# Optimization experiments

Hardware: AMD Instinct MI355X
Metric: run time of the kernel (lower is better)

Reference implementation:

```python
import jax, jax.numpy as jnp
import numpy as np

N_NODES = 100000
N_EDGES = 1600000
N_GRAPHS = 1024
IN_FEATS = 74
HID = 100


def setup_inputs() -> dict:
    key = jax.random.key(0)
    ks = jax.random.split(key, 16)
    node_feats = jax.random.normal(ks[0], (N_NODES, IN_FEATS), dtype=jnp.float32)
    src = jax.random.randint(ks[1], (N_EDGES,), 0, N_NODES, dtype=jnp.int32)
    dst = jax.random.randint(ks[2], (N_EDGES,), 0, N_NODES, dtype=jnp.int32)
    graph_ids = jnp.sort(jax.random.randint(ks[3], (N_NODES,), 0, N_GRAPHS, dtype=jnp.int32))

    def lin(k, fi, fo):
        s = 1.0 / np.sqrt(fi)
        kw, kb = jax.random.split(k)
        return (jax.random.uniform(kw, (fi, fo), jnp.float32, -s, s),
                jax.random.uniform(kb, (fo,), jnp.float32, -s, s))

    W_self1, _ = lin(ks[4], IN_FEATS, HID)
    W_neigh1, b1 = lin(ks[5], IN_FEATS, HID)
    W_self2, _ = lin(ks[6], HID, HID)
    W_neigh2, b2 = lin(ks[7], HID, HID)
    w_atom, b_atom = lin(ks[8], HID, 1)
    W_p1, b_p1 = lin(ks[9], 2 * HID, 64)
    W_p2, b_p2 = lin(ks[10], 64, 1)
    return {
        'node_feats': node_feats, 'src': src, 'dst': dst, 'graph_ids': graph_ids,
        'n_graphs': N_GRAPHS,
        'W_self1': W_self1, 'W_neigh1': W_neigh1, 'b1': b1,
        'W_self2': W_self2, 'W_neigh2': W_neigh2, 'b2': b2,
        'w_atom': w_atom, 'b_atom': b_atom,
        'W_p1': W_p1, 'b_p1': b_p1, 'W_p2': W_p2, 'b_p2': b_p2,
    }


def _sage_mean_layer(h, src, dst, W_self, W_neigh, b):
    # DGL SAGEConv, aggregator 'mean': out = h @ W_self + mean_{u->v}(h_u) @ W_neigh + b
    n = h.shape[0]
    msg = h[src]  # [E, F] gather
    agg = jax.ops.segment_sum(msg, dst, num_segments=n)
    deg = jax.ops.segment_sum(jnp.ones((src.shape[0],), h.dtype), dst, num_segments=n)
    h_neigh = agg / jnp.maximum(deg, 1.0)[:, None]
    return jax.nn.relu(h @ W_self + h_neigh @ W_neigh + b)


def reference(node_feats, src, dst, graph_ids, n_graphs,
              W_self1, W_neigh1, b1, W_self2, W_neigh2, b2,
              w_atom, b_atom, W_p1, b_p1, W_p2, b_p2):
    h = _sage_mean_layer(node_feats, src, dst, W_self1, W_neigh1, b1)
    h = _sage_mean_layer(h, src, dst, W_self2, W_neigh2, b2)

    # WeightedSumAndMax readout
    w = jax.nn.sigmoid(h @ w_atom + b_atom)          # [N, 1]
    g_sum = jax.ops.segment_sum(h * w, graph_ids, num_segments=n_graphs)   # [G, HID]
    g_max = jax.ops.segment_max(h, graph_ids, num_segments=n_graphs)       # [G, HID]
    g_max = jnp.where(jnp.isneginf(g_max), 0.0, g_max)  # empty graphs -> 0
    g_feats = jnp.concatenate([g_sum, g_max], axis=-1)  # [G, 2*HID]

    # MLP predictor: Linear(200,64) -> Linear(64,1) (no activation between)
    out = (g_feats @ W_p1 + b_p1) @ W_p2 + b_p2
    return out
```

## Files before the change

### kernel.cpp

```cpp
#include <hip/hip_runtime.h>

#define N_NODES 100000
#define N_PAD   100096
#define N_EDGES 1600000
#define N_GRAPHS 1024
#define F_IN 74
#define HID 100

#define KP1 160
#define KP2 224

#define FBF_LD 80
#define F8T_LD 80
#define AGT_LD 80
#define AGT2_LD 112
#define H1C8_LD 128
#define H2_LD  100

#define ZROW N_NODES

#define NB ((N_NODES + 255) / 256)
#define BKCAP 8192
#define BIN_EPB 4096
#define NBB ((N_EDGES + BIN_EPB - 1) / BIN_EPB)

typedef __attribute__((ext_vector_type(8))) short short8;
typedef __attribute__((ext_vector_type(4))) float f32x4;
typedef __attribute__((ext_vector_type(2))) float f32x2;

#if defined(__has_builtin)
#if __has_builtin(__builtin_amdgcn_cvt_pk_f32_fp8) && __has_builtin(__builtin_amdgcn_cvt_pk_fp8_f32)
#define HAVE_FP8 1
#endif
#endif

__device__ __forceinline__ unsigned short f2bf(float x) {
    union { float f; unsigned u; } c; c.f = x;
    unsigned u = c.u;
    unsigned r = (u + 0x7fffu + ((u >> 16) & 1u)) >> 16;
    return (unsigned short)r;
}
__device__ __forceinline__ float bf2f(unsigned short h) {
    union { unsigned u; float f; } c; c.u = ((unsigned)h) << 16;
    return c.f;
}
__device__ __forceinline__ float blo(unsigned w) { return bf2f((unsigned short)(w & 0xffffu)); }
__device__ __forceinline__ float bhi(unsigned w) { return bf2f((unsigned short)(w >> 16)); }
__device__ __forceinline__ unsigned bpack(float a, float b) {
    return (unsigned)f2bf(a) | ((unsigned)f2bf(b) << 16);
}
__device__ __forceinline__ void store8(void* p, unsigned lo, unsigned hi) {
    unsigned long long v = (unsigned long long)lo | ((unsigned long long)hi << 32);
    *(unsigned long long*)p = v;
}

__device__ __forceinline__ unsigned char enc_fp8_1(float v) {
#ifdef HAVE_FP8
    return (unsigned char)__builtin_amdgcn_cvt_pk_fp8_f32(v, 0.f, 0, false);
#else
    unsigned sgn = v < 0.f ? 0x80u : 0u;
    float m = fabsf(v);
    unsigned char mag;
    if (m < 0.015625f) {
        int q = (int)(m * 512.0f + 0.5f);
        mag = (unsigned char)(q > 7 ? 7 : q);
    } else {
        union { float f; unsigned u; } c; c.f = m;
        unsigned r = c.u + 0x7ffff + ((c.u >> 20) & 1u);
        int e = (int)(r >> 23) - 127;
        mag = (e > 8) ? (unsigned char)0x7e : (unsigned char)(((e + 7) << 3) | ((r >> 20) & 7u));
    }
    return (unsigned char)(sgn | mag);
#endif
}
__device__ __forceinline__ unsigned enc_fp8x4(float v0, float v1, float v2, float v3) {
#ifdef HAVE_FP8
    int r = __builtin_amdgcn_cvt_pk_fp8_f32(v0, v1, 0, false);
    r = __builtin_amdgcn_cvt_pk_fp8_f32(v2, v3, r, true);
    return (unsigned)r;
#else
    return (unsigned)enc_fp8_1(v0) | ((unsigned)enc_fp8_1(v1) << 8) |
           ((unsigned)enc_fp8_1(v2) << 16) | ((unsigned)enc_fp8_1(v3) << 24);
#endif
}
__device__ __forceinline__ void dec_fp8x4(unsigned w, float& x0, float& x1, float& x2, float& x3) {
#ifdef HAVE_FP8
    f32x2 lo = __builtin_amdgcn_cvt_pk_f32_fp8((int)w, false);
    f32x2 hi = __builtin_amdgcn_cvt_pk_f32_fp8((int)w, true);
    x0 = lo.x; x1 = lo.y; x2 = hi.x; x3 = hi.y;
#else
    auto d1 = [](unsigned b) -> float {
        float s = (b & 0x80u) ? -1.f : 1.f;
        b &= 0x7fu;
        if (b < 8) return s * (float)b * 0.001953125f;
        union { unsigned u; float f; } c;
        c.u = ((((b >> 3) & 15u) - 7 + 127) << 23) | ((b & 7u) << 20);
        return s * c.f;
    };
    x0 = d1(w & 0xffu); x1 = d1((w >> 8) & 0xffu);
    x2 = d1((w >> 16) & 0xffu); x3 = d1(w >> 24);
#endif
}
__device__ __forceinline__ short8 dec8bf(uint2 v) {
    float x0, x1, x2, x3, y0, y1, y2, y3;
    dec_fp8x4(v.x, x0, x1, x2, x3);
    dec_fp8x4(v.y, y0, y1, y2, y3);
    union { short8 s; unsigned u[4]; } r;
    r.u[0] = bpack(x0, x1); r.u[1] = bpack(x2, x3);
    r.u[2] = bpack(y0, y1); r.u[3] = bpack(y2, y3);
    return r.s;
}


__global__ __launch_bounds__(256) void k_bin(const int* __restrict__ src,
                                             const int* __restrict__ dst,
                                             int* __restrict__ bucket_fill,
                                             unsigned* __restrict__ bbuf) {
    __shared__ int cnt[NB];
    __shared__ int base[NB];
    int t = threadIdx.x;
    for (int i = t; i < NB; i += 256) cnt[i] = 0;
    __syncthreads();
    int e0 = blockIdx.x * BIN_EPB;
    int e1 = e0 + BIN_EPB < N_EDGES ? e0 + BIN_EPB : N_EDGES;
    for (int e = e0 + t; e < e1; e += 256) {
        atomicAdd(&cnt[dst[e] >> 8], 1);
    }
    __syncthreads();
    for (int i = t; i < NB; i += 256) {
        int c = cnt[i];
        base[i] = c ? atomicAdd(&bucket_fill[i], c) : 0;
        cnt[i] = 0;
    }
    __syncthreads();
    for (int e = e0 + t; e < e1; e += 256) {
        int d = dst[e];
        int b = d >> 8;
        int pos = atomicAdd(&cnt[b], 1);
        bbuf[(size_t)b * BKCAP + base[b] + pos] = ((unsigned)src[e] << 8) | (unsigned)(d & 255);
    }
}

__global__ __launch_bounds__(256) void k_scatter(const unsigned* __restrict__ bbuf,
                                                 const int* __restrict__ bucket_fill,
                                                 int2* __restrict__ rp2,
                                                 int* __restrict__ csr) {
    __shared__ int fc[256];
    __shared__ int ofs[256];
    __shared__ int wsum[4];
    int b = blockIdx.x, t = threadIdx.x;
    int nstart = b << 8;
    int base = b * BKCAP;
    int bend = base + bucket_fill[b];
    fc[t] = 0;
    __syncthreads();
    for (int i = base + t; i < bend; i += 256)
        atomicAdd(&fc[bbuf[i] & 255u], 1);
    __syncthreads();
    int d = fc[t];
    int dp = (d + 7) & ~7;
    int lane = t & 63, w = t >> 6;
    int inc = dp;
    #pragma unroll
    for (int o = 1; o < 64; o <<= 1) {
        int x = __shfl_up(inc, o, 64);
        if (lane >= o) inc += x;
    }
    if (lane == 63) wsum[w] = inc;
    __syncthreads();
    int woff = 0;
    for (int i = 0; i < w; ++i) woff += wsum[i];
    ofs[t] = base + woff + inc - dp;
    __syncthreads();
    int node = nstart + t;
    int o0 = ofs[t];
    if (node < N_NODES) rp2[node] = make_int2(o0, o0 + d);
    for (int i = o0 + d; i < o0 + dp; ++i) csr[i] = ZROW;
    fc[t] = 0;
    __syncthreads();
    for (int i = base + t; i < bend; i += 256) {
        unsigned p = bbuf[i];
        int dl = (int)(p & 255u);
        int pos = atomicAdd(&fc[dl], 1);
        csr[ofs[dl] + pos] = (int)(p >> 8);
    }
}


__global__ void k_feats(const float* __restrict__ feats, short* __restrict__ fbf,
                        unsigned* __restrict__ f8t, unsigned* __restrict__ h1c8) {
    int idx = blockIdx.x * blockDim.x + threadIdx.x;
    if (idx < H1C8_LD / 4) h1c8[(size_t)ZROW * (H1C8_LD / 4) + idx] = 0u;
    if (idx >= (N_NODES + 1) * (F8T_LD / 4)) return;
    int n = idx / (F8T_LD / 4), g = idx - n * (F8T_LD / 4);
    int c0 = 4 * g;
    float v0 = 0.f, v1 = 0.f, v2 = 0.f, v3 = 0.f;
    if (n < N_NODES) {
        const float* r = feats + (size_t)n * F_IN;
        v0 = (c0 + 0 < F_IN) ? r[c0 + 0] : 0.f;
        v1 = (c0 + 1 < F_IN) ? r[c0 + 1] : 0.f;
        v2 = (c0 + 2 < F_IN) ? r[c0 + 2] : 0.f;
        v3 = (c0 + 3 < F_IN) ? r[c0 + 3] : 0.f;
    }
    unsigned* fb = (unsigned*)fbf + (size_t)n * (FBF_LD / 2) + 2 * g;
    fb[0] = bpack(v0, v1);
    fb[1] = bpack(v2, v3);
    f8t[idx] = enc_fp8x4(v0, v1, v2, v3);
}


template <int KP, int K1, int AGG0>
__global__ void k_wconv(const float* __restrict__ Ws, const float* __restrict__ Wn,
                        short* __restrict__ Whi, short* __restrict__ Wlo) {
    int idx = blockIdx.x * blockDim.x + threadIdx.x;
    if (idx >= 112 * KP) return;
    int col = idx / KP, k = idx - col * KP;
    float v = 0.f;
    if (col < HID) {
        if (k < K1) v = Ws[k * HID + col];
        else if (k >= AGG0 && k < AGG0 + K1) v = Wn[(k - AGG0) * HID + col];
    }
    unsigned short hi = f2bf(v);
    unsigned short lo = f2bf(v - bf2f(hi));
    Whi[idx] = (short)hi;
    Wlo[idx] = (short)lo;
}


__global__ __launch_bounds__(256) void k_prep1(const unsigned char* __restrict__ f8t,
                        const int2* __restrict__ rp2, const int* __restrict__ csr,
                        short* __restrict__ agt) {
    int wid = threadIdx.x >> 6, lane = threadIdx.x & 63;
    int v = blockIdx.x * 4 + wid;
    if (v >= N_NODES) return;
    int h = lane >> 5, q = lane & 31;
    int2 se = rp2[v];
    int s = se.x, e = se.y;
    int deg = e - s;
    int pe = s + ((deg + 7) & ~7);
    float a0 = 0.f, a1 = 0.f, a2 = 0.f, a3 = 0.f;
    if (q < 19) {
        #pragma unroll 2
        for (int j = s; j < pe; j += 8) {
            unsigned w0 = *(const unsigned*)(f8t + (size_t)csr[j + h] * F8T_LD + q * 4);
            unsigned w1 = *(const unsigned*)(f8t + (size_t)csr[j + 2 + h] * F8T_LD + q * 4);
            unsigned w2 = *(const unsigned*)(f8t + (size_t)csr[j + 4 + h] * F8T_LD + q * 4);
            unsigned w3 = *(const unsigned*)(f8t + (size_t)csr[j + 6 + h] * F8T_LD + q * 4);
            float x0, x1, x2, x3;
            dec_fp8x4(w0, x0, x1, x2, x3); a0 += x0; a1 += x1; a2 += x2; a3 += x3;
            dec_fp8x4(w1, x0, x1, x2, x3); a0 += x0; a1 += x1; a2 += x2; a3 += x3;
            dec_fp8x4(w2, x0, x1, x2, x3); a0 += x0; a1 += x1; a2 += x2; a3 += x3;
            dec_fp8x4(w3, x0, x1, x2, x3); a0 += x0; a1 += x1; a2 += x2; a3 += x3;
        }
    }
    a0 += __shfl_xor(a0, 32, 64);
    a1 += __shfl_xor(a1, 32, 64);
    a2 += __shfl_xor(a2, 32, 64);
    a3 += __shfl_xor(a3, 32, 64);
    float inv = 1.0f / fmaxf((float)deg, 1.0f);
    if (h == 0 && q < 20) {
        store8((char*)agt + (size_t)v * (AGT_LD * 2) + q * 8,
               bpack(a0 * inv, a1 * inv), bpack(a2 * inv, a3 * inv));
    }
}


__global__ __launch_bounds__(256) void k_prep2(const unsigned char* __restrict__ h1c8,
                        const int2* __restrict__ rp2, const int* __restrict__ csr,
                        short* __restrict__ agt2) {
    int wid = threadIdx.x >> 6, lane = threadIdx.x & 63;
    int v = blockIdx.x * 4 + wid;
    if (v >= N_NODES) return;
    int h = lane >> 5, q = lane & 31;
    int2 se = rp2[v];
    int s = se.x, e = se.y;
    int deg = e - s;
    int pe = s + ((deg + 7) & ~7);
    float a0 = 0.f, a1 = 0.f, a2 = 0.f, a3 = 0.f;
    if (q < 25) {
        #pragma unroll 2
        for (int j = s; j < pe; j += 8) {
            unsigned w0 = *(const unsigned*)(h1c8 + (size_t)csr[j + h] * H1C8_LD + q * 4);
            unsigned w1 = *(const unsigned*)(h1c8 + (size_t)csr[j + 2 + h] * H1C8_LD + q * 4);
            unsigned w2 = *(const unsigned*)(h1c8 + (size_t)csr[j + 4 + h] * H1C8_LD + q * 4);
            unsigned w3 = *(const unsigned*)(h1c8 + (size_t)csr[j + 6 + h] * H1C8_LD + q * 4);
            float x0, x1, x2, x3;
            dec_fp8x4(w0, x0, x1, x2, x3); a0 += x0; a1 += x1; a2 += x2; a3 += x3;
            dec_fp8x4(w1, x0, x1, x2, x3); a0 += x0; a1 += x1; a2 += x2; a3 += x3;
            dec_fp8x4(w2, x0, x1, x2, x3); a0 += x0; a1 += x1; a2 += x2; a3 += x3;
            dec_fp8x4(w3, x0, x1, x2, x3); a0 += x0; a1 += x1; a2 += x2; a3 += x3;
        }
    }
    a0 += __shfl_xor(a0, 32, 64);
    a1 += __shfl_xor(a1, 32, 64);
    a2 += __shfl_xor(a2, 32, 64);
    a3 += __shfl_xor(a3, 32, 64);
    float inv = 1.0f / fmaxf((float)deg, 1.0f);
    char* Aw = (char*)agt2 + (size_t)v * (AGT2_LD * 2);
    if (h == 0 && q < 25) {
        store8(Aw + q * 8, bpack(a0 * inv, a1 * inv), bpack(a2 * inv, a3 * inv));
    }
    if (h == 1 && q < 3) {
        store8(Aw + 200 + q * 8, 0u, 0u);
    }
}


__global__ __launch_bounds__(128) void k_mfma1(
    const short* __restrict__ fbf, const short* __restrict__ agt,
    const short* __restrict__ Wthi, const short* __restrict__ Wtlo,
    const float* __restrict__ bias, unsigned char* __restrict__ h1c8) {
    int t = threadIdx.x;
    int wid = t >> 6, lane = t & 63;
    int quad = lane >> 4, lr = lane & 15;
    int rowbase = blockIdx.x * 64 + wid * 32;

    short8 ap[2][5];
    #pragma unroll
    for (int rf = 0; rf < 2; ++rf) {
        int row = rowbase + rf * 16 + lr;
        #pragma unroll
        for (int c = 0; c < 5; ++c) {
            const short* p;
            if (c < 2) p = fbf + (size_t)row * FBF_LD + c * 32 + quad * 8;
            else if (c == 2) p = (quad < 2) ? fbf + (size_t)row * FBF_LD + 64 + quad * 8
                                            : agt + (size_t)row * AGT_LD + (quad - 2) * 8;
            else p = agt + (size_t)row * AGT_LD + (c - 3) * 32 + 16 + quad * 8;
            ap[rf][c] = *(const short8*)p;
        }
    }

    f32x4 acc[2][7];
    #pragma unroll
    for (int rf = 0; rf < 2; ++rf)
        #pragma unroll
        for (int n = 0; n < 7; ++n) acc[rf][n] = (f32x4){0.f, 0.f, 0.f, 0.f};

    #pragma unroll
    for (int c = 0; c < 5; ++c) {
        #pragma unroll
        for (int n = 0; n < 7; ++n) {
            size_t off = (size_t)(n * 16 + lr) * KP1 + c * 32 + quad * 8;
            short8 wh = *(const short8*)(Wthi + off);
            short8 wl = *(const short8*)(Wtlo + off);
            #pragma unroll
            for (int rf = 0; rf < 2; ++rf) {
                acc[rf][n] = __builtin_amdgcn_mfma_f32_16x16x32_bf16(ap[rf][c], wh, acc[rf][n], 0, 0, 0);
                acc[rf][n] = __builtin_amdgcn_mfma_f32_16x16x32_bf16(ap[rf][c], wl, acc[rf][n], 0, 0, 0);
            }
        }
    }

    #pragma unroll
    for (int rf = 0; rf < 2; ++rf) {
        #pragma unroll
        for (int n = 0; n < 7; ++n) {
            int col = n * 16 + lr;
            float bv = (col < HID) ? bias[col] : 0.f;
            #pragma unroll
            for (int r = 0; r < 4; ++r) {
                int row = rowbase + rf * 16 + quad * 4 + r;
                if (row < N_NODES) {
                    unsigned char enc = 0;
                    if (col < HID) enc = enc_fp8_1(fmaxf(acc[rf][n][r] + bv, 0.f));
                    h1c8[(size_t)row * H1C8_LD + col] = enc;
                }
            }
        }
        #pragma unroll
        for (int r = 0; r < 4; ++r) {
            int row = rowbase + rf * 16 + quad * 4 + r;
            if (row < N_NODES) h1c8[(size_t)row * H1C8_LD + 112 + lr] = 0;
        }
    }
}


__global__ __launch_bounds__(128) void k_mfma2(
    const unsigned char* __restrict__ h1c8, const short* __restrict__ agt2,
    const short* __restrict__ Wthi, const short* __restrict__ Wtlo,
    const float* __restrict__ bias, const float* __restrict__ w_atom,
    const float* __restrict__ b_atom,
    short* __restrict__ h2c, float* __restrict__ aw) {
    int t = threadIdx.x;
    int wid = t >> 6, lane = t & 63;
    int quad = lane >> 4, lr = lane & 15;
    int rowbase = blockIdx.x * 64 + wid * 32;

    short8 ap[2][7];
    #pragma unroll
    for (int rf = 0; rf < 2; ++rf) {
        int row = rowbase + rf * 16 + lr;
        const unsigned char* hr = h1c8 + (size_t)row * H1C8_LD;
        const short* ar = agt2 + (size_t)row * AGT2_LD;
        #pragma unroll
        for (int c = 0; c < 7; ++c) {
            if (c < 3) {
                ap[rf][c] = dec8bf(*(const uint2*)(hr + c * 32 + quad * 8));
            } else if (c == 3) {
                if (quad < 2) ap[rf][c] = dec8bf(*(const uint2*)(hr + 96 + quad * 8));
                else ap[rf][c] = *(const short8*)(ar + (quad - 2) * 8);
            } else {
                ap[rf][c] = *(const short8*)(ar + (c - 4) * 32 + 16 + quad * 8);
            }
        }
    }

    f32x4 acc[2][7];
    #pragma unroll
    for (int rf = 0; rf < 2; ++rf)
        #pragma unroll
        for (int n = 0; n < 7; ++n) acc[rf][n] = (f32x4){0.f, 0.f, 0.f, 0.f};

    #pragma unroll
    for (int c = 0; c < 7; ++c) {
        #pragma unroll
        for (int n = 0; n < 7; ++n) {
            size_t off = (size_t)(n * 16 + lr) * KP2 + c * 32 + quad * 8;
            short8 wh = *(const short8*)(Wthi + off);
            short8 wl = *(const short8*)(Wtlo + off);
            #pragma unroll
            for (int rf = 0; rf < 2; ++rf) {
                acc[rf][n] = __builtin_amdgcn_mfma_f32_16x16x32_bf16(ap[rf][c], wh, acc[rf][n], 0, 0, 0);
                acc[rf][n] = __builtin_amdgcn_mfma_f32_16x16x32_bf16(ap[rf][c], wl, acc[rf][n], 0, 0, 0);
            }
        }
    }

    float ba = b_atom[0];
    #pragma unroll
    for (int rf = 0; rf < 2; ++rf) {
        float dotr0 = 0.f, dotr1 = 0.f, dotr2 = 0.f, dotr3 = 0.f;
        #pragma unroll
        for (int n = 0; n < 7; ++n) {
            int col = n * 16 + lr;
            if (col < HID) {
                float bv = bias[col];
                float wa = w_atom[col];
                #pragma unroll
                for (int r = 0; r < 4; ++r) {
                    int row = rowbase + rf * 16 + quad * 4 + r;
                    if (row < N_NODES) {
                        float v = fmaxf(acc[rf][n][r] + bv, 0.f);
                        h2c[(size_t)row * H2_LD + col] = (short)f2bf(v);
                        float dv = v * wa;
                        if (r == 0) dotr0 += dv;
                        else if (r == 1) dotr1 += dv;
                        else if (r == 2) dotr2 += dv;
                        else dotr3 += dv;
                    }
                }
            }
        }
        #pragma unroll
        for (int off = 1; off < 16; off <<= 1) {
            dotr0 += __shfl_xor(dotr0, off, 64);
            dotr1 += __shfl_xor(dotr1, off, 64);
            dotr2 += __shfl_xor(dotr2, off, 64);
            dotr3 += __shfl_xor(dotr3, off, 64);
        }
        if (lr == 0) {
            int row0 = rowbase + rf * 16 + quad * 4;
            float d[4] = {dotr0, dotr1, dotr2, dotr3};
            #pragma unroll
            for (int r = 0; r < 4; ++r) {
                int row = row0 + r;
                if (row < N_NODES) aw[row] = 1.f / (1.f + __expf(-(d[r] + ba)));
            }
        }
    }
}


__global__ void k_weff(const float* __restrict__ Wp1, const float* __restrict__ bp1,
                       const float* __restrict__ Wp2, const float* __restrict__ bp2,
                       float* __restrict__ weff) {
    int t = threadIdx.x;
    if (t < 200) {
        float s = 0.f;
        for (int k = 0; k < 64; ++k) s += Wp1[t * 64 + k] * Wp2[k];
        weff[t] = s;
    } else if (t == 200) {
        float s = bp2[0];
        for (int k = 0; k < 64; ++k) s += bp1[k] * Wp2[k];
        weff[200] = s;
    }
}


__global__ __launch_bounds__(256) void k_readout(
    const unsigned short* __restrict__ h2c, const float* __restrict__ aw,
    const int* __restrict__ graph_ids, const float* __restrict__ weff,
    float* __restrict__ out) {
    int g = blockIdx.x;
    int t = threadIdx.x, lane = t & 63, w = t >> 6;

    int s_, e_;
    {
        int l = 0, r = N_NODES;
        while (l < r) { int m = (l + r) >> 1; if (graph_ids[m] < g) l = m + 1; else r = m; }
        s_ = l;
        l = s_; r = N_NODES;
        while (l < r) { int m = (l + r) >> 1; if (graph_ids[m] < g + 1) l = m + 1; else r = m; }
        e_ = l;
    }

    float sum0 = 0.f, sum1 = 0.f, mx0 = 0.f, mx1 = 0.f;
    for (int i = s_ + w; i < e_; i += 4) {
        float wt = aw[i];
        if (lane < 50) {
            unsigned wv = *(const unsigned*)(h2c + (size_t)i * H2_LD + 2 * lane);
            float v0 = blo(wv), v1 = bhi(wv);
            sum0 += v0 * wt;
            sum1 += v1 * wt;
            mx0 = fmaxf(mx0, v0);
            mx1 = fmaxf(mx1, v1);
        }
    }

    __shared__ float ssum[4][HID];
    __shared__ float smx[4][HID];
    if (lane < 50) {
        ssum[w][2 * lane] = sum0;
        ssum[w][2 * lane + 1] = sum1;
        smx[w][2 * lane] = mx0;
        smx[w][2 * lane + 1] = mx1;
    }
    __syncthreads();

    float contrib = 0.f;
    if (t < HID) {
        float sumf = ssum[0][t] + ssum[1][t] + ssum[2][t] + ssum[3][t];
        float mxf = fmaxf(fmaxf(smx[0][t], smx[1][t]), fmaxf(smx[2][t], smx[3][t]));
        contrib = sumf * weff[t] + mxf * weff[HID + t];
    }
    #pragma unroll
    for (int off = 32; off; off >>= 1) contrib += __shfl_xor(contrib, off, 64);
    __shared__ float red[4];
    if (lane == 0) red[w] = contrib;
    __syncthreads();
    if (t == 0) out[g] = red[0] + red[1] + red[2] + red[3] + weff[200];
}


extern "C" void kernel_launch(void* const* d_in, const int* in_sizes, int n_in,
                              void* d_out, int out_size, void* d_ws, size_t ws_size,
                              hipStream_t stream) {
    const float* node_feats = (const float*)d_in[0];
    const int* src = (const int*)d_in[1];
    const int* dst = (const int*)d_in[2];
    const int* gid = (const int*)d_in[3];
    const float* Ws1 = (const float*)d_in[5];
    const float* Wn1 = (const float*)d_in[6];
    const float* b1 = (const float*)d_in[7];
    const float* Ws2 = (const float*)d_in[8];
    const float* Wn2 = (const float*)d_in[9];
    const float* b2 = (const float*)d_in[10];
    const float* w_atom = (const float*)d_in[11];
    const float* b_atom = (const float*)d_in[12];
    const float* Wp1 = (const float*)d_in[13];
    const float* bp1 = (const float*)d_in[14];
    const float* Wp2 = (const float*)d_in[15];
    const float* bp2 = (const float*)d_in[16];
    float* out = (float*)d_out;

    char* ws = (char*)d_ws;
    size_t off = 0;
    auto alloc = [&](size_t bytes) -> void* {
        void* p = (void*)(ws + off);
        off += (bytes + 255) & ~(size_t)255;
        return p;
    };
    int2* rp2 = (int2*)alloc((size_t)N_NODES * sizeof(int2));
    int* bucket_fill = (int*)alloc(NB * sizeof(int));
    int* csr = (int*)alloc((size_t)NB * BKCAP * sizeof(int));
    unsigned* bbuf = (unsigned*)alloc((size_t)NB * BKCAP * sizeof(unsigned));
    short* fbf = (short*)alloc((size_t)(N_PAD + 1) * FBF_LD * sizeof(short));
    unsigned char* f8t = (unsigned char*)alloc((size_t)(N_PAD + 1) * F8T_LD);
    short* agt = (short*)alloc((size_t)N_PAD * AGT_LD * sizeof(short));
    short* agt2 = (short*)alloc((size_t)N_PAD * AGT2_LD * sizeof(short));
    unsigned char* h1c8 = (unsigned char*)alloc((size_t)(N_NODES + 1) * H1C8_LD);
    short* h2c = (short*)alloc((size_t)N_NODES * H2_LD * sizeof(short));
    float* aw = (float*)alloc((size_t)N_NODES * sizeof(float));
    short* Wt1hi = (short*)alloc(112 * KP1 * sizeof(short));
    short* Wt1lo = (short*)alloc(112 * KP1 * sizeof(short));
    short* Wt2hi = (short*)alloc(112 * KP2 * sizeof(short));
    short* Wt2lo = (short*)alloc(112 * KP2 * sizeof(short));
    float* weff = (float*)alloc(256 * sizeof(float));

    hipMemsetAsync(bucket_fill, 0, NB * sizeof(int), stream);

    k_bin<<<NBB, 256, 0, stream>>>(src, dst, bucket_fill, bbuf);
    k_scatter<<<NB, 256, 0, stream>>>(bbuf, bucket_fill, rp2, csr);

    k_feats<<<((N_NODES + 1) * (F8T_LD / 4) + 255) / 256, 256, 0, stream>>>(
        node_feats, fbf, (unsigned*)f8t, (unsigned*)h1c8);
    k_wconv<KP1, F_IN, 80><<<(112 * KP1 + 255) / 256, 256, 0, stream>>>(Ws1, Wn1, Wt1hi, Wt1lo);
    k_wconv<KP2, HID, 112><<<(112 * KP2 + 255) / 256, 256, 0, stream>>>(Ws2, Wn2, Wt2hi, Wt2lo);

    k_prep1<<<(N_NODES + 3) / 4, 256, 0, stream>>>(f8t, rp2, csr, agt);
    k_mfma1<<<N_PAD / 64, 128, 0, stream>>>(fbf, agt, Wt1hi, Wt1lo, b1, h1c8);
    k_prep2<<<(N_NODES + 3) / 4, 256, 0, stream>>>(h1c8, rp2, csr, agt2);
    k_mfma2<<<N_PAD / 64, 128, 0, stream>>>(h1c8, agt2, Wt2hi, Wt2lo, b2, w_atom, b_atom, h2c, aw);

    k_weff<<<1, 256, 0, stream>>>(Wp1, bp1, Wp2, bp2, weff);
    k_readout<<<N_GRAPHS, 256, 0, stream>>>((const unsigned short*)h2c, aw, gid, weff, out);
}
```

Baseline: 248.8 us.

## Split MFMA GEMM kernels across two column-half blocks per row tile

Each row tile of both dense layer kernels is now processed by two blocks. One block computes output column groups 0-3 and the other groups 4-6, which doubles the grid and cuts accumulator registers per thread. Because the atom-weight dot product is now split, each half writes its partial sum, and the readout adds the two partials plus the bias before applying the sigmoid. In exchange, the A-operand rows are loaded and decoded twice and an extra partial buffer has to be read.

```diff
diff --git a/kernel.cpp b/kernel.cpp
--- a/kernel.cpp
+++ b/kernel.cpp
@@ -311,9 +311,12 @@
     const short* __restrict__ Wthi, const short* __restrict__ Wtlo,
     const float* __restrict__ bias, unsigned char* __restrict__ h1c8) {
     int t = threadIdx.x;
+    int nh = blockIdx.x & 1, rb = blockIdx.x >> 1;
+    const int NG = nh ? 3 : 4;
+    const int ng0 = nh ? 4 : 0;
     int wid = t >> 6, lane = t & 63;
     int quad = lane >> 4, lr = lane & 15;
-    int rowbase = blockIdx.x * 64 + wid * 32;
+    int rowbase = rb * 64 + wid * 32;
 
     short8 ap[2][5];
     #pragma unroll
@@ -330,23 +333,25 @@
         }
     }
 
-    f32x4 acc[2][7];
+    f32x4 acc[2][4];
     #pragma unroll
     for (int rf = 0; rf < 2; ++rf)
         #pragma unroll
-        for (int n = 0; n < 7; ++n) acc[rf][n] = (f32x4){0.f, 0.f, 0.f, 0.f};
+        for (int n = 0; n < 4; ++n) acc[rf][n] = (f32x4){0.f, 0.f, 0.f, 0.f};
 
     #pragma unroll
     for (int c = 0; c < 5; ++c) {
         #pragma unroll
-        for (int n = 0; n < 7; ++n) {
-            size_t off = (size_t)(n * 16 + lr) * KP1 + c * 32 + quad * 8;
-            short8 wh = *(const short8*)(Wthi + off);
-            short8 wl = *(const short8*)(Wtlo + off);
-            #pragma unroll
-            for (int rf = 0; rf < 2; ++rf) {
-                acc[rf][n] = __builtin_amdgcn_mfma_f32_16x16x32_bf16(ap[rf][c], wh, acc[rf][n], 0, 0, 0);
-                acc[rf][n] = __builtin_amdgcn_mfma_f32_16x16x32_bf16(ap[rf][c], wl, acc[rf][n], 0, 0, 0);
+        for (int n = 0; n < 4; ++n) {
+            if (n < NG) {
+                size_t off = (size_t)((ng0 + n) * 16 + lr) * KP1 + c * 32 + quad * 8;
+                short8 wh = *(const short8*)(Wthi + off);
+                short8 wl = *(const short8*)(Wtlo + off);
+                #pragma unroll
+                for (int rf = 0; rf < 2; ++rf) {
+                    acc[rf][n] = __builtin_amdgcn_mfma_f32_16x16x32_bf16(ap[rf][c], wh, acc[rf][n], 0, 0, 0);
+                    acc[rf][n] = __builtin_amdgcn_mfma_f32_16x16x32_bf16(ap[rf][c], wl, acc[rf][n], 0, 0, 0);
+                }
             }
         }
     }
@@ -354,23 +359,27 @@
     #pragma unroll
     for (int rf = 0; rf < 2; ++rf) {
         #pragma unroll
-        for (int n = 0; n < 7; ++n) {
-            int col = n * 16 + lr;
-            float bv = (col < HID) ? bias[col] : 0.f;
+        for (int n = 0; n < 4; ++n) {
+            if (n < NG) {
+                int col = (ng0 + n) * 16 + lr;
+                float bv = (col < HID) ? bias[col] : 0.f;
+                #pragma unroll
+                for (int r = 0; r < 4; ++r) {
+                    int row = rowbase + rf * 16 + quad * 4 + r;
+                    if (row < N_NODES) {
+                        unsigned char enc = 0;
+                        if (col < HID) enc = enc_fp8_1(fmaxf(acc[rf][n][r] + bv, 0.f));
+                        h1c8[(size_t)row * H1C8_LD + col] = enc;
+                    }
+                }
+            }
+        }
+        if (nh == 1) {
             #pragma unroll
             for (int r = 0; r < 4; ++r) {
                 int row = rowbase + rf * 16 + quad * 4 + r;
-                if (row < N_NODES) {
-                    unsigned char enc = 0;
-                    if (col < HID) enc = enc_fp8_1(fmaxf(acc[rf][n][r] + bv, 0.f));
-                    h1c8[(size_t)row * H1C8_LD + col] = enc;
-                }
+                if (row < N_NODES) h1c8[(size_t)row * H1C8_LD + 112 + lr] = 0;
             }
-        }
-        #pragma unroll
-        for (int r = 0; r < 4; ++r) {
-            int row = rowbase + rf * 16 + quad * 4 + r;
-            if (row < N_NODES) h1c8[(size_t)row * H1C8_LD + 112 + lr] = 0;
         }
     }
 }
@@ -380,12 +389,14 @@
     const unsigned char* __restrict__ h1c8, const short* __restrict__ agt2,
     const short* __restrict__ Wthi, const short* __restrict__ Wtlo,
     const float* __restrict__ bias, const float* __restrict__ w_atom,
-    const float* __restrict__ b_atom,
-    short* __restrict__ h2c, float* __restrict__ aw) {
+    short* __restrict__ h2c, float* __restrict__ awp) {
     int t = threadIdx.x;
+    int nh = blockIdx.x & 1, rb = blockIdx.x >> 1;
+    const int NG = nh ? 3 : 4;
+    const int ng0 = nh ? 4 : 0;
     int wid = t >> 6, lane = t & 63;
     int quad = lane >> 4, lr = lane & 15;
-    int rowbase = blockIdx.x * 64 + wid * 32;
+    int rowbase = rb * 64 + wid * 32;
 
     short8 ap[2][7];
     #pragma unroll
@@ -406,48 +417,51 @@
         }
     }
 
-    f32x4 acc[2][7];
+    f32x4 acc[2][4];
     #pragma unroll
     for (int rf = 0; rf < 2; ++rf)
         #pragma unroll
-        for (int n = 0; n < 7; ++n) acc[rf][n] = (f32x4){0.f, 0.f, 0.f, 0.f};
+        for (int n = 0; n < 4; ++n) acc[rf][n] = (f32x4){0.f, 0.f, 0.f, 0.f};
 
     #pragma unroll
     for (int c = 0; c < 7; ++c) {
         #pragma unroll
-        for (int n = 0; n < 7; ++n) {
-            size_t off = (size_t)(n * 16 + lr) * KP2 + c * 32 + quad * 8;
-            short8 wh = *(const short8*)(Wthi + off);
-            short8 wl = *(const short8*)(Wtlo + off);
-            #pragma unroll
-            for (int rf = 0; rf < 2; ++rf) {
-                acc[rf][n] = __builtin_amdgcn_mfma_f32_16x16x32_bf16(ap[rf][c], wh, acc[rf][n], 0, 0, 0);
-                acc[rf][n] = __builtin_amdgcn_mfma_f32_16x16x32_bf16(ap[rf][c], wl, acc[rf][n], 0, 0, 0);
+        for (int n = 0; n < 4; ++n) {
+            if (n < NG) {
+                size_t off = (size_t)((ng0 + n) * 16 + lr) * KP2 + c * 32 + quad * 8;
+                short8 wh = *(const short8*)(Wthi + off);
+                short8 wl = *(const short8*)(Wtlo + off);
+                #pragma unroll
+                for (int rf = 0; rf < 2; ++rf) {
+                    acc[rf][n] = __builtin_amdgcn_mfma_f32_16x16x32_bf16(ap[rf][c], wh, acc[rf][n], 0, 0, 0);
+                    acc[rf][n] = __builtin_amdgcn_mfma_f32_16x16x32_bf16(ap[rf][c], wl, acc[rf][n], 0, 0, 0);
+                }
             }
         }
     }
 
-    float ba = b_atom[0];
     #pragma unroll
     for (int rf = 0; rf < 2; ++rf) {
         float dotr0 = 0.f, dotr1 = 0.f, dotr2 = 0.f, dotr3 = 0.f;
         #pragma unroll
-        for (int n = 0; n < 7; ++n) {
-            int col = n * 16 + lr;
-            if (col < HID) {
-                float bv = bias[col];
-                float wa = w_atom[col];
-                #pragma unroll
-                for (int r = 0; r < 4; ++r) {
-                    int row = rowbase + rf * 16 + quad * 4 + r;
-                    if (row < N_NODES) {
-                        float v = fmaxf(acc[rf][n][r] + bv, 0.f);
-                        h2c[(size_t)row * H2_LD + col] = (short)f2bf(v);
-                        float dv = v * wa;
-                        if (r == 0) dotr0 += dv;
-                        else if (r == 1) dotr1 += dv;
-                        else if (r == 2) dotr2 += dv;
-                        else dotr3 += dv;
+        for (int n = 0; n < 4; ++n) {
+            if (n < NG) {
+                int col = (ng0 + n) * 16 + lr;
+                if (col < HID) {
+                    float bv = bias[col];
+                    float wa = w_atom[col];
+                    #pragma unroll
+                    for (int r = 0; r < 4; ++r) {
+                        int row = rowbase + rf * 16 + quad * 4 + r;
+                        if (row < N_NODES) {
+                            float v = fmaxf(acc[rf][n][r] + bv, 0.f);
+                            h2c[(size_t)row * H2_LD + col] = (short)f2bf(v);
+                            float dv = v * wa;
+                            if (r == 0) dotr0 += dv;
+                            else if (r == 1) dotr1 += dv;
+                            else if (r == 2) dotr2 += dv;
+                            else dotr3 += dv;
+                        }
                     }
                 }
             }
@@ -465,7 +479,7 @@
             #pragma unroll
             for (int r = 0; r < 4; ++r) {
                 int row = row0 + r;
-                if (row < N_NODES) aw[row] = 1.f / (1.f + __expf(-(d[r] + ba)));
+                if (row < N_NODES) awp[(size_t)nh * N_NODES + row] = d[r];
             }
         }
     }
@@ -489,9 +503,9 @@
 
 
 __global__ __launch_bounds__(256) void k_readout(
-    const unsigned short* __restrict__ h2c, const float* __restrict__ aw,
+    const unsigned short* __restrict__ h2c, const float* __restrict__ awp,
     const int* __restrict__ graph_ids, const float* __restrict__ weff,
-    float* __restrict__ out) {
+    const float* __restrict__ b_atom, float* __restrict__ out) {
     int g = blockIdx.x;
     int t = threadIdx.x, lane = t & 63, w = t >> 6;
 
@@ -505,9 +519,10 @@
         e_ = l;
     }
 
+    float ba = b_atom[0];
     float sum0 = 0.f, sum1 = 0.f, mx0 = 0.f, mx1 = 0.f;
     for (int i = s_ + w; i < e_; i += 4) {
-        float wt = aw[i];
+        float wt = 1.f / (1.f + __expf(-(awp[i] + awp[N_NODES + i] + ba)));
         if (lane < 50) {
             unsigned wv = *(const unsigned*)(h2c + (size_t)i * H2_LD + 2 * lane);
             float v0 = blo(wv), v1 = bhi(wv);
@@ -581,7 +596,7 @@
     short* agt2 = (short*)alloc((size_t)N_PAD * AGT2_LD * sizeof(short));
     unsigned char* h1c8 = (unsigned char*)alloc((size_t)(N_NODES + 1) * H1C8_LD);
     short* h2c = (short*)alloc((size_t)N_NODES * H2_LD * sizeof(short));
-    float* aw = (float*)alloc((size_t)N_NODES * sizeof(float));
+    float* awp = (float*)alloc((size_t)2 * N_NODES * sizeof(float));
     short* Wt1hi = (short*)alloc(112 * KP1 * sizeof(short));
     short* Wt1lo = (short*)alloc(112 * KP1 * sizeof(short));
     short* Wt2hi = (short*)alloc(112 * KP2 * sizeof(short));
@@ -599,10 +614,10 @@
     k_wconv<KP2, HID, 112><<<(112 * KP2 + 255) / 256, 256, 0, stream>>>(Ws2, Wn2, Wt2hi, Wt2lo);
 
     k_prep1<<<(N_NODES + 3) / 4, 256, 0, stream>>>(f8t, rp2, csr, agt);
-    k_mfma1<<<N_PAD / 64, 128, 0, stream>>>(fbf, agt, Wt1hi, Wt1lo, b1, h1c8);
+    k_mfma1<<<(N_PAD / 64) * 2, 128, 0, stream>>>(fbf, agt, Wt1hi, Wt1lo, b1, h1c8);
     k_prep2<<<(N_NODES + 3) / 4, 256, 0, stream>>>(h1c8, rp2, csr, agt2);
-    k_mfma2<<<N_PAD / 64, 128, 0, stream>>>(h1c8, agt2, Wt2hi, Wt2lo, b2, w_atom, b_atom, h2c, aw);
+    k_mfma2<<<(N_PAD / 64) * 2, 128, 0, stream>>>(h1c8, agt2, Wt2hi, Wt2lo, b2, w_atom, h2c, awp);
 
     k_weff<<<1, 256, 0, stream>>>(Wp1, bp1, Wp2, bp2, weff);
-    k_readout<<<N_GRAPHS, 256, 0, stream>>>((const unsigned short*)h2c, aw, gid, weff, out);
-}
+    k_readout<<<N_GRAPHS, 256, 0, stream>>>((const unsigned short*)h2c, awp, gid, weff, b_atom, out);
+}
```

Result: faster. 237.6 us (median of 2 runs) (-4.5%).
